# Optimization experiments

Measured on AMD Instinct MI355X. Metric: run time of the kernel, lower is better.

The kernel has to match this reference:

```python
import jax, jax.numpy as jnp
import numpy as np

B, C, H, W = 8, 8, 512, 512

# one-pixel shifts with zero padding (equivalent to the bmm with shift matrices)
def shift_right(x):  # out[..., c] = x[..., c-1]
    return jnp.pad(x, ((0, 0), (0, 0), (1, 0)))[:, :, :-1]
def shift_left(x):   # out[..., c] = x[..., c+1]
    return jnp.pad(x, ((0, 0), (0, 0), (0, 1)))[:, :, 1:]
def shift_up(x):     # out[r] = x[r+1]
    return jnp.pad(x, ((0, 0), (0, 1), (0, 0)))[:, 1:, :]
def shift_down(x):   # out[r] = x[r-1]
    return jnp.pad(x, ((0, 0), (1, 0), (0, 0)))[:, :-1, :]

def bilater_voting(c):
    # c: [B, 8, H, W] probabilities
    right        = shift_right(c[:, 4])
    left         = shift_left(c[:, 3])
    left_bottom  = shift_left(shift_down(c[:, 5]))
    right_above  = shift_right(shift_up(c[:, 2]))
    left_above   = shift_left(shift_up(c[:, 0]))
    bottom       = shift_down(c[:, 6])
    up           = shift_up(c[:, 1])
    right_bottom = shift_right(shift_down(c[:, 7]))
    a1 = c[:, 3] * right
    a2 = c[:, 4] * left
    a3 = c[:, 1] * bottom
    a4 = c[:, 6] * up
    a5 = c[:, 2] * left_bottom
    a6 = c[:, 5] * right_above
    a7 = c[:, 0] * right_bottom
    a8 = c[:, 7] * left_above
    vote_out = jnp.stack([a7, a3, a5, a1, a2, a6, a4, a8], axis=1)
    glo_map = jnp.mean(vote_out, axis=1)
    return glo_map, vote_out

def bce(p, t):
    # matches torch F.binary_cross_entropy (mean reduction, log clamped at -100)
    logp = jnp.clip(jnp.log(p), -100.0, None)
    log1mp = jnp.clip(jnp.log(1.0 - p), -100.0, None)
    return -jnp.mean(t * logp + (1.0 - t) * log1mp)

def setup_inputs() -> dict:
    key = jax.random.key(0)
    k1, k2, k3, k4 = jax.random.split(key, 4)
    atts = jax.random.normal(k1, (B, C, H, W), dtype=jnp.float32)
    dets = jax.random.normal(k2, (B, C, H, W), dtype=jnp.float32)
    target = jax.random.randint(k3, (B, 1, H, W), 0, 2).astype(jnp.float32)
    con_target = jax.random.randint(k4, (B, C, H, W), 0, 2).astype(jnp.float32)
    return {"atts": atts, "dets": dets, "target": target, "con_target": con_target}

def reference(atts, dets, target, con_target):
    # edge mask from connectivity GT: pixels with 0 < sum < 8
    sum_conn = jnp.sum(con_target, axis=1)  # [B, H, W]
    edge_conn = jnp.where((sum_conn < 8.0) & (sum_conn > 0.0), 1.0, 0.0)

    atts_p = jax.nn.sigmoid(atts)
    dets_p = jax.nn.sigmoid(dets)

    glo_map1, vote_out1 = bilater_voting(atts_p)
    glo_map2, vote_out2 = bilater_voting(dets_p)

    # edge/decouple loss on dets branch
    pred_mask_min = 1.0 - jnp.min(vote_out2, axis=1)
    pred_mask_min = pred_mask_min * edge_conn
    decouple_map = glo_map2 * (1.0 - edge_conn) + pred_mask_min
    de_loss2 = bce(decouple_map[:, None], target)

    bce_loss1 = bce(glo_map1[:, None], target)
    bicon_loss1 = bce(vote_out1, con_target)
    conn_loss1 = bce(atts_p, con_target)
    bicon_loss2 = bce(vote_out2, con_target)
    conn_loss2 = bce(dets_p, con_target)

    loss = (0.2 * bicon_loss1 + 0.8 * conn_loss1 + bce_loss1
            + 0.2 * bicon_loss2 + 0.8 * conn_loss2 + de_loss2)
    return loss
```

## Files before the change

kernel.cpp:

```cpp
#include <hip/hip_runtime.h>

#define BB 8
#define CC 8
#define HH 512
#define WW 512
#define HWSZ (HH * WW)
#define CHW (CC * HWSZ)

typedef float v4 __attribute__((ext_vector_type(4)));

#define LOG2_CLAMP -144.26950409f

__device__ __forceinline__ float sigf(float x) {
    return __builtin_amdgcn_rcpf(1.0f + __expf(-x));
}

__device__ __forceinline__ void stage_rows(const float* __restrict__ base,
                                           float* __restrict__ lds,
                                           int h, int hm, int hp,
                                           int rgrp, int col4)
{
#pragma unroll
    for (int j = 0; j < 4; ++j) {
        int row = j * 4 + rgrp;
        if (row < 14) {
            int ch, grow;
            if (row < 8)       { ch = row;      grow = h;  }
            else if (row < 11) { ch = row - 3;  grow = hm; }
            else               { ch = row - 11; grow = hp; }
            v4 d = *(const v4* __restrict__)(base + ch * HWSZ + grow * WW + col4);
            *(v4*)(lds + row * WW + col4) = d;
        }
    }
}

template <bool NEED_MIN>
__device__ __forceinline__ void eval_lds(const float* __restrict__ L, int w,
                                         float mh0, float mh1,
                                         const float* __restrict__ cv,
                                         float& glo, float& vmin,
                                         float& Lbic, float& Lcon)
{
    const int wl = (w > 0) ? w - 1 : 0;
    const int wr = (w < WW - 1) ? w + 1 : WW - 1;
    const float mw0 = (w > 0) ? 1.0f : 0.0f;
    const float mw1 = (w < WW - 1) ? 1.0f : 0.0f;

    float s[8];
#pragma unroll
    for (int c = 0; c < 8; ++c) s[c] = sigf(L[c * WW + w]);

    float n[8];
    n[0] = sigf(L[10 * WW + wl]) * (mh0 * mw0);
    n[1] = sigf(L[ 9 * WW + w ]) *  mh0;
    n[2] = sigf(L[ 8 * WW + wr]) * (mh0 * mw1);
    n[3] = sigf(L[ 4 * WW + wl]) *  mw0;
    n[4] = sigf(L[ 3 * WW + wr]) *  mw1;
    n[5] = sigf(L[13 * WW + wl]) * (mh1 * mw0);
    n[6] = sigf(L[12 * WW + w ]) *  mh1;
    n[7] = sigf(L[11 * WW + wr]) * (mh1 * mw1);

    float pb0 = 1.f, pb1 = 1.f, pc = 1.f, vsum = 0.f;
    if (NEED_MIN) vmin = 1e30f;
#pragma unroll
    for (int k = 0; k < 8; ++k) {
        float v = s[k] * n[k];
        vsum += v;
        if (NEED_MIN) vmin = fminf(vmin, v);
        float t  = cv[k];
        float av = (t > 0.5f) ? v    : 1.0f - v;
        float as = (t > 0.5f) ? s[k] : 1.0f - s[k];
        if (k < 4) pb0 *= av; else pb1 *= av;
        pc *= as;
    }
    glo  = vsum * 0.125f;
    Lbic = fmaxf(__log2f(pb0), LOG2_CLAMP) + fmaxf(__log2f(pb1), LOG2_CLAMP);
    Lcon = fmaxf(__log2f(pc), LOG2_CLAMP);
}

__global__ __launch_bounds__(512, 8) void bicon_loss_kernel(
    const float* __restrict__ atts, const float* __restrict__ dets,
    const float* __restrict__ target, const float* __restrict__ con,
    float* __restrict__ out)
{
    __shared__ float L[14 * WW];
    __shared__ float wsum[8];

    const int t   = threadIdx.x;
    const int row = blockIdx.x;
    const int h   = row & (HH - 1);
    const int b   = row >> 9;
    const int w   = t;

    const int   hm  = (h > 0)      ? h - 1 : 0;
    const int   hp  = (h < HH - 1) ? h + 1 : HH - 1;
    const float mh0 = (h > 0)      ? 1.0f : 0.0f;
    const float mh1 = (h < HH - 1) ? 1.0f : 0.0f;

    const float* __restrict__ ab = atts + b * CHW;
    const float* __restrict__ db = dets + b * CHW;

    const float* __restrict__ cb = con + b * CHW + h * WW + w;
    float cv[8];
#pragma unroll
    for (int c = 0; c < 8; ++c) cv[c] = cb[c * HWSZ];
    const float tt = target[b * HWSZ + h * WW + w];

    const int rgrp = t >> 7;
    const int col4 = (t & 127) << 2;

    stage_rows(ab, L, h, hm, hp, rgrp, col4);
    __syncthreads();
    float glo1, dum, Lb1, Lc1;
    eval_lds<false>(L, w, mh0, mh1, cv, glo1, dum, Lb1, Lc1);
    __syncthreads();

    stage_rows(db, L, h, hm, hp, rgrp, col4);
    __syncthreads();
    float glo2, vmin2, Lb2, Lc2;
    eval_lds<true>(L, w, mh0, mh1, cv, glo2, vmin2, Lb2, Lc2);

    float csum = 0.f;
#pragma unroll
    for (int c = 0; c < 8; ++c) csum += cv[c];
    const float edge = (csum < 8.0f && csum > 0.0f) ? 1.0f : 0.0f;

    const float dec = (edge > 0.5f) ? (1.0f - vmin2) : glo2;
    const float a   = (tt > 0.5f) ? glo1 : 1.0f - glo1;
    const float bs  = (tt > 0.5f) ? dec  : 1.0f - dec;
    const float Lp  = fmaxf(__log2f(a * bs), LOG2_CLAMP);

    const float wbic = 0.2f / (float)(BB * CC * HWSZ);
    const float wcon = 0.8f / (float)(BB * CC * HWSZ);
    const float wpix = 1.0f / (float)(BB * HWSZ);
    const float ln2  = 0.69314718056f;

    float local = -(wbic * (Lb1 + Lb2) + wcon * (Lc1 + Lc2) + wpix * Lp) * ln2;

#pragma unroll
    for (int off = 32; off > 0; off >>= 1)
        local += __shfl_down(local, off, 64);

    const int lane = t & 63;
    const int wid  = t >> 6;
    if (lane == 0) wsum[wid] = local;
    __syncthreads();
    if (t == 0) {
        float s = 0.f;
#pragma unroll
        for (int i = 0; i < 8; ++i) s += wsum[i];
        atomicAdd(out, s);
    }
}

extern "C" void kernel_launch(void* const* d_in, const int* in_sizes, int n_in,
                              void* d_out, int out_size, void* d_ws, size_t ws_size,
                              hipStream_t stream) {
    const float* atts   = (const float*)d_in[0];
    const float* dets   = (const float*)d_in[1];
    const float* target = (const float*)d_in[2];
    const float* con    = (const float*)d_in[3];
    float* out = (float*)d_out;

    hipMemsetAsync(out, 0, sizeof(float), stream);

    bicon_loss_kernel<<<BB * HH, 512, 0, stream>>>(atts, dets, target, con, out);
}
```

Baseline: 210.5 us.

## Stage only neighbor rows in LDS for both branches at once, load centers directly

Only the eight neighbor rows each branch actually needs (two from the current row, three from above, three from below) go to shared memory, staged for atts and dets together in one pass. The centre-pixel channel values are now read directly into registers with coalesced global loads. This removes one staging round and two block barriers, and lets all global loads be issued before the single sync so more memory traffic is in flight. In exchange it uses more registers and LDS (16 rows instead of 14), which may reduce occupancy.

After: 206.0 us. 2.1% less time.

```diff
diff --git a/kernel.cpp b/kernel.cpp
--- a/kernel.cpp
+++ b/kernel.cpp
@@ -15,50 +15,26 @@
     return __builtin_amdgcn_rcpf(1.0f + __expf(-x));
 }
 
-__device__ __forceinline__ void stage_rows(const float* __restrict__ base,
-                                           float* __restrict__ lds,
-                                           int h, int hm, int hp,
-                                           int rgrp, int col4)
+template <bool NEED_MIN>
+__device__ __forceinline__ void eval_branch(
+    const float* __restrict__ Lb, const float* __restrict__ craw,
+    int w, int wl, int wr, float mh0, float mh1, float mw0, float mw1,
+    const float* __restrict__ cv,
+    float& glo, float& vmin, float& Lbic, float& Lcon)
 {
-#pragma unroll
-    for (int j = 0; j < 4; ++j) {
-        int row = j * 4 + rgrp;
-        if (row < 14) {
-            int ch, grow;
-            if (row < 8)       { ch = row;      grow = h;  }
-            else if (row < 11) { ch = row - 3;  grow = hm; }
-            else               { ch = row - 11; grow = hp; }
-            v4 d = *(const v4* __restrict__)(base + ch * HWSZ + grow * WW + col4);
-            *(v4*)(lds + row * WW + col4) = d;
-        }
-    }
-}
-
-template <bool NEED_MIN>
-__device__ __forceinline__ void eval_lds(const float* __restrict__ L, int w,
-                                         float mh0, float mh1,
-                                         const float* __restrict__ cv,
-                                         float& glo, float& vmin,
-                                         float& Lbic, float& Lcon)
-{
-    const int wl = (w > 0) ? w - 1 : 0;
-    const int wr = (w < WW - 1) ? w + 1 : WW - 1;
-    const float mw0 = (w > 0) ? 1.0f : 0.0f;
-    const float mw1 = (w < WW - 1) ? 1.0f : 0.0f;
-
     float s[8];
 #pragma unroll
-    for (int c = 0; c < 8; ++c) s[c] = sigf(L[c * WW + w]);
+    for (int c = 0; c < 8; ++c) s[c] = sigf(craw[c]);
 
     float n[8];
-    n[0] = sigf(L[10 * WW + wl]) * (mh0 * mw0);
-    n[1] = sigf(L[ 9 * WW + w ]) *  mh0;
-    n[2] = sigf(L[ 8 * WW + wr]) * (mh0 * mw1);
-    n[3] = sigf(L[ 4 * WW + wl]) *  mw0;
-    n[4] = sigf(L[ 3 * WW + wr]) *  mw1;
-    n[5] = sigf(L[13 * WW + wl]) * (mh1 * mw0);
-    n[6] = sigf(L[12 * WW + w ]) *  mh1;
-    n[7] = sigf(L[11 * WW + wr]) * (mh1 * mw1);
+    n[0] = sigf(Lb[4 * WW + wl]) * (mh0 * mw0);
+    n[1] = sigf(Lb[3 * WW + w ]) *  mh0;
+    n[2] = sigf(Lb[2 * WW + wr]) * (mh0 * mw1);
+    n[3] = sigf(Lb[1 * WW + wl]) *  mw0;
+    n[4] = sigf(Lb[0 * WW + wr]) *  mw1;
+    n[5] = sigf(Lb[7 * WW + wl]) * (mh1 * mw0);
+    n[6] = sigf(Lb[6 * WW + w ]) *  mh1;
+    n[7] = sigf(Lb[5 * WW + wr]) * (mh1 * mw1);
 
     float pb0 = 1.f, pb1 = 1.f, pc = 1.f, vsum = 0.f;
     if (NEED_MIN) vmin = 1e30f;
@@ -83,7 +59,7 @@
     const float* __restrict__ target, const float* __restrict__ con,
     float* __restrict__ out)
 {
-    __shared__ float L[14 * WW];
+    __shared__ float L[16 * WW];
     __shared__ float wsum[8];
 
     const int t   = threadIdx.x;
@@ -96,29 +72,50 @@
     const int   hp  = (h < HH - 1) ? h + 1 : HH - 1;
     const float mh0 = (h > 0)      ? 1.0f : 0.0f;
     const float mh1 = (h < HH - 1) ? 1.0f : 0.0f;
+    const int   wl  = (w > 0)      ? w - 1 : 0;
+    const int   wr  = (w < WW - 1) ? w + 1 : WW - 1;
+    const float mw0 = (w > 0)      ? 1.0f : 0.0f;
+    const float mw1 = (w < WW - 1) ? 1.0f : 0.0f;
 
     const float* __restrict__ ab = atts + b * CHW;
     const float* __restrict__ db = dets + b * CHW;
-
-    const float* __restrict__ cb = con + b * CHW + h * WW + w;
-    float cv[8];
-#pragma unroll
-    for (int c = 0; c < 8; ++c) cv[c] = cb[c * HWSZ];
-    const float tt = target[b * HWSZ + h * WW + w];
+    const int offC = h * WW + w;
 
     const int rgrp = t >> 7;
     const int col4 = (t & 127) << 2;
 
-    stage_rows(ab, L, h, hm, hp, rgrp, col4);
-    __syncthreads();
-    float glo1, dum, Lb1, Lc1;
-    eval_lds<false>(L, w, mh0, mh1, cv, glo1, dum, Lb1, Lc1);
+    v4 stg[4];
+#pragma unroll
+    for (int j = 0; j < 4; ++j) {
+        const int rr = rgrp + 4 * (j & 1);
+        const int ch   = (rr < 5) ? rr + 3 : rr - 5;
+        const int grow = (rr < 2) ? h : ((rr < 5) ? hm : hp);
+        const float* base = (j < 2) ? ab : db;
+        stg[j] = *(const v4* __restrict__)(base + ch * HWSZ + grow * WW + col4);
+    }
+
+    float cv[8];
+#pragma unroll
+    for (int c = 0; c < 8; ++c) cv[c] = con[b * CHW + c * HWSZ + offC];
+    const float tt = target[b * HWSZ + offC];
+    float ar[8], dr[8];
+#pragma unroll
+    for (int c = 0; c < 8; ++c) ar[c] = ab[c * HWSZ + offC];
+#pragma unroll
+    for (int c = 0; c < 8; ++c) dr[c] = db[c * HWSZ + offC];
+
+#pragma unroll
+    for (int j = 0; j < 4; ++j) {
+        const int r = rgrp + 4 * (j & 1) + ((j < 2) ? 0 : 8);
+        *(v4*)(L + r * WW + col4) = stg[j];
+    }
     __syncthreads();
 
-    stage_rows(db, L, h, hm, hp, rgrp, col4);
-    __syncthreads();
-    float glo2, vmin2, Lb2, Lc2;
-    eval_lds<true>(L, w, mh0, mh1, cv, glo2, vmin2, Lb2, Lc2);
+    float glo1, glo2, vmin2, dum, Lb1, Lc1, Lb2, Lc2;
+    eval_branch<false>(L,           ar, w, wl, wr, mh0, mh1, mw0, mw1, cv,
+                       glo1, dum, Lb1, Lc1);
+    eval_branch<true >(L + 8 * WW,  dr, w, wl, wr, mh0, mh1, mw0, mw1, cv,
+                       glo2, vmin2, Lb2, Lc2);
 
     float csum = 0.f;
 #pragma unroll
```
